# Kernel optimization log

Hardware: AMD Instinct MI355X
Metric: run time of the kernel (lower is better)

The kernel has to match this reference:

```python
import jax, jax.numpy as jnp
import numpy as np

S, I = 512, 384
C_MSA, C_Z, H, C = 64, 128, 8, 32
EPS = 1e-5


def _layernorm(x, g, b):
    mu = jnp.mean(x, axis=-1, keepdims=True)
    var = jnp.var(x, axis=-1, keepdims=True)
    return (x - mu) * jax.lax.rsqrt(var + EPS) * g + b


def setup_inputs() -> dict:
    key = jax.random.key(0)
    ks = jax.random.split(key, 6)
    sc_v = 1.0 / np.sqrt(C_MSA)
    sc_z = 1.0 / np.sqrt(C_Z)
    sc_o = 1.0 / np.sqrt(H * C)
    return {
        "msa_SI": jax.random.normal(ks[0], (S, I, C_MSA), jnp.float32),
        "pair_II": jax.random.normal(ks[1], (I, I, C_Z), jnp.float32),
        "ln_msa_g": jnp.ones((C_MSA,), jnp.float32),
        "ln_msa_b": jnp.zeros((C_MSA,), jnp.float32),
        "ln_pair_g": jnp.ones((C_Z,), jnp.float32),
        "ln_pair_b": jnp.zeros((C_Z,), jnp.float32),
        "W_v": jax.random.normal(ks[2], (C_MSA, H * C), jnp.float32) * sc_v,
        "W_bias": jax.random.normal(ks[3], (C_Z, H), jnp.float32) * sc_z,
        "W_gate": jax.random.normal(ks[4], (C_MSA, H * C), jnp.float32) * sc_v,
        "W_out": jax.random.normal(ks[5], (H * C, C_MSA), jnp.float32) * sc_o,
    }


def reference(msa_SI, pair_II, ln_msa_g, ln_msa_b, ln_pair_g, ln_pair_b,
              W_v, W_bias, W_gate, W_out):
    s, i = msa_SI.shape[:2]
    msa_n = _layernorm(msa_SI, ln_msa_g, ln_msa_b)              # [S,I,Cm]
    v_SIHC = (msa_n @ W_v).reshape(s, i, H, C)                   # [S,I,H,C]
    bias_IIH = _layernorm(pair_II, ln_pair_g, ln_pair_b) @ W_bias  # [I,I,H]
    w_IIH = jax.nn.softmax(bias_IIH, axis=-2)                    # softmax over j
    gate = jax.nn.sigmoid(msa_n @ W_gate)                        # [S,I,H*C]
    # weighted average shared across S: [I,I,H] x [S,I,H,C] -> [S,I,H,C]
    weights = jnp.einsum('ijh,sjhc->sihc', w_IIH, v_SIHC).reshape(s, i, H * C)
    o = gate * weights
    return o @ W_out                                             # [S,I,Cm]
```

## Files before the change

### kernel.cpp

```cpp
#include <hip/hip_runtime.h>
#include <hip/hip_bf16.h>

#define S_DIM 512
#define I_DIM 384
#define CM 64
#define CZ 128
#define H_DIM 8
#define C_DIM 32
#define HC 256
#define II (I_DIM*I_DIM)

typedef short bf16x8 __attribute__((ext_vector_type(8)));
typedef float f32x4 __attribute__((ext_vector_type(4)));

__device__ __forceinline__ float s2f(short s) {
    unsigned int u = ((unsigned int)(unsigned short)s) << 16;
    float f; __builtin_memcpy(&f, &u, 4); return f;
}
__device__ __forceinline__ short f2bf(float f) {
    __hip_bfloat16 h = __float2bfloat16(f);
    short r; __builtin_memcpy(&r, &h, 2); return r;
}

__device__ __forceinline__ void glds16(const short* g, short* l) {
    __builtin_amdgcn_global_load_lds(
        (const __attribute__((address_space(1))) void*)g,
        (__attribute__((address_space(3))) void*)l, 16, 0, 0);
}

__global__ __launch_bounds__(256) void k_pair_ln_bias(
    const float* __restrict__ pair, const float* __restrict__ g,
    const float* __restrict__ b, const float* __restrict__ Wb,
    float* __restrict__ bias)
{
    __shared__ float xs[4][CZ];
    __shared__ float WbT[H_DIM*132];
    const int tid = threadIdx.x;
    const int wv = tid >> 6, lane = tid & 63;
    const int ij = blockIdx.x*4 + wv;

    {
        float4 q = *(const float4*)(Wb + tid*4);
        int m = tid*4;
        WbT[(m&7)*132 + (m>>3)]     = q.x;
        WbT[((m+1)&7)*132 + ((m+1)>>3)] = q.y;
        WbT[((m+2)&7)*132 + ((m+2)>>3)] = q.z;
        WbT[((m+3)&7)*132 + ((m+3)>>3)] = q.w;
    }

    float2 x2 = *(const float2*)(pair + (size_t)ij*CZ + lane*2);
    float s1 = x2.x + x2.y;
    float s2 = x2.x*x2.x + x2.y*x2.y;
#pragma unroll
    for (int off = 32; off > 0; off >>= 1) {
        s1 += __shfl_xor(s1, off, 64);
        s2 += __shfl_xor(s2, off, 64);
    }
    float mu = s1 * (1.f/CZ);
    float var = s2 * (1.f/CZ) - mu*mu;
    float rs = rsqrtf(var + 1e-5f);
    xs[wv][lane*2]   = (x2.x - mu)*rs*g[lane*2]   + b[lane*2];
    xs[wv][lane*2+1] = (x2.y - mu)*rs*g[lane*2+1] + b[lane*2+1];
    __syncthreads();

    const int h = lane >> 3, seg = lane & 7;
    float p = 0.f;
#pragma unroll
    for (int jj = 0; jj < 16; jj++) {
        int c = seg + jj*8;
        p += xs[wv][c] * WbT[h*132 + c];
    }
    p += __shfl_down(p, 4, 64);
    p += __shfl_down(p, 2, 64);
    p += __shfl_down(p, 1, 64);
    if (seg == 0) bias[(size_t)h*II + ij] = p;
}

__global__ __launch_bounds__(384) void k_softmax(
    const float* __restrict__ bias, short* __restrict__ w)
{
    int blk = blockIdx.x;
    int i = blk >> 3, h = blk & 7;
    int j = threadIdx.x;
    float x = bias[(size_t)h*II + i*I_DIM + j];
    float m = x;
#pragma unroll
    for (int off = 32; off > 0; off >>= 1) m = fmaxf(m, __shfl_xor(m, off, 64));
    __shared__ float red[6];
    int wv = j >> 6;
    if ((j & 63) == 0) red[wv] = m;
    __syncthreads();
    m = red[0];
#pragma unroll
    for (int k = 1; k < 6; k++) m = fmaxf(m, red[k]);
    float e = __expf(x - m);
    float s = e;
#pragma unroll
    for (int off = 32; off > 0; off >>= 1) s += __shfl_xor(s, off, 64);
    __syncthreads();
    if ((j & 63) == 0) red[wv] = s;
    __syncthreads();
    s = 0.f;
#pragma unroll
    for (int k = 0; k < 6; k++) s += red[k];
    w[(size_t)h*II + i*I_DIM + j] = f2bf(e / s);
}

__global__ __launch_bounds__(256) void k_prep_w(
    const float* __restrict__ Wv, const float* __restrict__ Wg,
    const float* __restrict__ Wo,
    short* __restrict__ Wt, short* __restrict__ Wot)
{
    int idx = blockIdx.x*256 + threadIdx.x;
    if (idx < 512*64) {
        int n = idx >> 6, k = idx & 63;
        Wt[idx] = f2bf((n < HC) ? Wv[k*HC + n] : Wg[k*HC + (n - HC)]);
    } else {
        int q = idx - 512*64;
        int n = q >> 8, k = q & 255;
        Wot[q] = f2bf(Wo[k*64 + n]);
    }
}

__global__ __launch_bounds__(256) void k4_ln_vgate(
    const float* __restrict__ msa_c,
    const float* __restrict__ gm, const float* __restrict__ bm,
    const short* __restrict__ Wt,
    short* __restrict__ v_t, short* __restrict__ gate)
{
    __shared__ alignas(16) short lds[20992];
    short* As = lds;
    short* Bs = lds + 4608;
    short* T  = lds;

    const int tid = threadIdx.x;
    const int wave = tid >> 6;
    const int lane = tid & 63;
    const int pm = blockIdx.y;

    auto stage_b = [&](int kt) {
#pragma unroll
        for (int c2 = 0; c2 < 8; c2++)
            glds16(Wt + (size_t)(c2*64 + lane)*64 + kt*32 + wave*8,
                   &Bs[(wave*512 + c2*64)*8]);
    };
    stage_b(0);

    {
        const int row = tid >> 2;
        const int seg = tid & 3;
        float xf[16], gf[16], bf[16];
        const float* rp = msa_c + (size_t)(pm*64 + row)*CM + seg*16;
#pragma unroll
        for (int q = 0; q < 4; q++) {
            float4 a = *(const float4*)(rp + q*4);
            xf[q*4] = a.x; xf[q*4+1] = a.y; xf[q*4+2] = a.z; xf[q*4+3] = a.w;
            float4 gg = *(const float4*)(gm + seg*16 + q*4);
            gf[q*4] = gg.x; gf[q*4+1] = gg.y; gf[q*4+2] = gg.z; gf[q*4+3] = gg.w;
            float4 bb = *(const float4*)(bm + seg*16 + q*4);
            bf[q*4] = bb.x; bf[q*4+1] = bb.y; bf[q*4+2] = bb.z; bf[q*4+3] = bb.w;
        }
        float s1 = 0.f, s2 = 0.f;
#pragma unroll
        for (int j = 0; j < 16; j++) { s1 += xf[j]; s2 += xf[j]*xf[j]; }
        s1 += __shfl_xor(s1, 1); s2 += __shfl_xor(s2, 1);
        s1 += __shfl_xor(s1, 2); s2 += __shfl_xor(s2, 2);
        float mu = s1 * (1.f/64.f);
        float var = s2 * (1.f/64.f) - mu*mu;
        float rs = rsqrtf(var + 1e-5f);
        bf16x8 o0, o1;
#pragma unroll
        for (int j = 0; j < 8; j++) {
            o0[j] = f2bf((xf[j]   - mu)*rs*gf[j]   + bf[j]);
            o1[j] = f2bf((xf[8+j] - mu)*rs*gf[8+j] + bf[8+j]);
        }
        *(bf16x8*)&As[row*72 + seg*16]     = o0;
        *(bf16x8*)&As[row*72 + seg*16 + 8] = o1;
    }

    const int fr = lane & 15, fq = lane >> 4;
    f32x4 acc[4][8] = {};

    for (int kt = 0; kt < 2; ++kt) {
        __syncthreads();

        bf16x8 af[4], bfrag[8];
#pragma unroll
        for (int mi = 0; mi < 4; mi++)
            af[mi] = *(const bf16x8*)&As[(mi*16 + fr)*72 + kt*32 + fq*8];
#pragma unroll
        for (int ni = 0; ni < 8; ni++)
            bfrag[ni] = *(const bf16x8*)&Bs[(fq*512 + wave*128 + ni*16 + fr)*8];
#pragma unroll
        for (int mi = 0; mi < 4; mi++)
#pragma unroll
            for (int ni = 0; ni < 8; ni++)
                acc[mi][ni] = __builtin_amdgcn_mfma_f32_16x16x32_bf16(
                    af[mi], bfrag[ni], acc[mi][ni], 0, 0, 0);
        __syncthreads();
        if (kt == 0) stage_b(1);
    }

    const int s_local = pm / 6;
    const int j0 = (pm % 6) * 64;
    if (wave < 2) {
#pragma unroll
        for (int mi = 0; mi < 4; mi++)
#pragma unroll
        for (int ni = 0; ni < 8; ni++) {
            int cl = wave*128 + ni*16 + fr;
            short4 pk;
            pk.x = f2bf(acc[mi][ni][0]);
            pk.y = f2bf(acc[mi][ni][1]);
            pk.z = f2bf(acc[mi][ni][2]);
            pk.w = f2bf(acc[mi][ni][3]);
            *(short4*)&T[cl*72 + mi*16 + fq*4] = pk;
        }
    } else {
#pragma unroll
        for (int mi = 0; mi < 4; mi++)
#pragma unroll
        for (int ni = 0; ni < 8; ni++)
#pragma unroll
        for (int r = 0; r < 4; r++) {
            int rowg = pm*64 + mi*16 + fq*4 + r;
            int col = (wave - 2)*128 + ni*16 + fr;
            gate[(size_t)rowg*HC + col] =
                f2bf(1.f/(1.f + __expf(-acc[mi][ni][r])));
        }
    }
    __syncthreads();
#pragma unroll
    for (int p = 0; p < 8; p++) {
        int unit = p*256 + tid;
        int cl = unit >> 3, part = unit & 7;
        bf16x8 d = *(const bf16x8*)&T[cl*72 + part*8];
        int h = cl >> 5, cc = cl & 31;
        *(bf16x8*)&v_t[(((size_t)s_local*H_DIM + h)*C_DIM + cc)*I_DIM + j0 + part*8] = d;
    }
}

__global__ __launch_bounds__(256, 2) void k56_einsum_proj(
    const short* __restrict__ w,
    const short* __restrict__ v_t,
    const short* __restrict__ gate,
    const short* __restrict__ Wot,
    float* __restrict__ out)
{
    __shared__ alignas(16) short Ws[2][4*192*8];
    __shared__ alignas(16) short Vs[2][2][1024];
    __shared__ alignas(16) short Ob[4][96*40];
    const int tid = threadIdx.x;
    const int wave = tid >> 6, lane = tid & 63;
    const int fr = lane & 15, fq = lane >> 4;
    const int ibase = blockIdx.x * 192;
    const int sp = blockIdx.y;
    const int ms = wave >> 1;
    const int kv = wave & 1;
    const int s  = sp*2 + ms;
    const int iw = kv * 96;

    const short* vbm = v_t + (size_t)s * H_DIM * C_DIM * I_DIM;

    auto stage = [&](int h_, int kt_, int buf) {
        const short* wp = w + (size_t)h_*II + kt_*32 + wave*8;
#pragma unroll
        for (int rg = 0; rg < 3; rg++)
            glds16(wp + (size_t)(ibase + rg*64 + lane)*I_DIM,
                   &Ws[buf][(wave*192 + rg*64)*8]);
        glds16(vbm + (size_t)h_*C_DIM*I_DIM + (lane & 31)*I_DIM + kt_*32
                   + (2*kv + (lane >> 5))*8,
               &Vs[buf][ms][kv*512]);
    };

    f32x4 acc_o[6][4] = {};

    stage(0, 0, 0);
    stage(0, 1, 1);

    for (int h = 0; h < H_DIM; h++) {
        f32x4 acc_e[2][6] = {};
        short4 gv[2][6];
        bf16x8 bw[4];
#pragma unroll
        for (int kt = 0; kt < 12; kt++) {
            const int cb = kt & 1;
            asm volatile("s_waitcnt vmcnt(4)" ::: "memory");
            __builtin_amdgcn_s_barrier();
            __builtin_amdgcn_sched_barrier(0);

            bf16x8 av[2], bwv[6];
#pragma unroll
            for (int mi = 0; mi < 2; mi++)
                av[mi] = *(const bf16x8*)&Vs[cb][ms][(fq*32 + mi*16 + fr)*8];
#pragma unroll
            for (int ni = 0; ni < 6; ni++)
                bwv[ni] = *(const bf16x8*)&Ws[cb][(fq*192 + iw + ni*16 + fr)*8];
            asm volatile("s_waitcnt lgkmcnt(0)" ::: "memory");
            __builtin_amdgcn_s_barrier();
            __builtin_amdgcn_sched_barrier(0);

            if (kt == 10) {
#pragma unroll
                for (int ni = 0; ni < 4; ni++)
                    bw[ni] = *(const bf16x8*)&Wot[(ni*16 + fr)*HC + h*C_DIM + fq*8];
#pragma unroll
                for (int mi = 0; mi < 2; mi++)
#pragma unroll
                for (int ni = 0; ni < 6; ni++)
                    gv[mi][ni] = *(const short4*)&gate[
                        (size_t)(s*I_DIM + ibase + iw + ni*16 + fr)*HC
                        + h*C_DIM + mi*16 + fq*4];
            }
            if (kt < 10)          stage(h, kt + 2, cb);
            else if (h < 7)       stage(h + 1, kt - 10, cb);

            __builtin_amdgcn_s_setprio(1);
#pragma unroll
            for (int mi = 0; mi < 2; mi++)
#pragma unroll
                for (int ni = 0; ni < 6; ni++)
                    acc_e[mi][ni] = __builtin_amdgcn_mfma_f32_16x16x32_bf16(
                        av[mi], bwv[ni], acc_e[mi][ni], 0, 0, 0);
            __builtin_amdgcn_s_setprio(0);
        }

        short* myOb = Ob[wave];
#pragma unroll
        for (int mi = 0; mi < 2; mi++)
#pragma unroll
        for (int ni = 0; ni < 6; ni++) {
            int row = ni*16 + fr;
            int c0 = mi*16 + fq*4;
            short4 g = gv[mi][ni];
            short4 pk;
            pk.x = f2bf(acc_e[mi][ni][0] * s2f(g.x));
            pk.y = f2bf(acc_e[mi][ni][1] * s2f(g.y));
            pk.z = f2bf(acc_e[mi][ni][2] * s2f(g.z));
            pk.w = f2bf(acc_e[mi][ni][3] * s2f(g.w));
            *(short4*)&myOb[row*40 + c0] = pk;
        }
        bf16x8 ao[6];
#pragma unroll
        for (int mi = 0; mi < 6; mi++)
            ao[mi] = *(const bf16x8*)&myOb[(mi*16 + fr)*40 + fq*8];
        __builtin_amdgcn_s_setprio(1);
#pragma unroll
        for (int mi = 0; mi < 6; mi++)
#pragma unroll
            for (int ni = 0; ni < 4; ni++)
                acc_o[mi][ni] = __builtin_amdgcn_mfma_f32_16x16x32_bf16(
                    ao[mi], bw[ni], acc_o[mi][ni], 0, 0, 0);
        __builtin_amdgcn_s_setprio(0);
    }

#pragma unroll
    for (int mi = 0; mi < 6; mi++)
#pragma unroll
    for (int ni = 0; ni < 4; ni++)
#pragma unroll
    for (int r = 0; r < 4; r++) {
        int i = ibase + iw + mi*16 + fq*4 + r;
        int n = ni*16 + fr;
        out[(size_t)(s*I_DIM + i)*CM + n] = acc_o[mi][ni][r];
    }
}

extern "C" void kernel_launch(void* const* d_in, const int* in_sizes, int n_in,
                              void* d_out, int out_size, void* d_ws, size_t ws_size,
                              hipStream_t stream)
{
    const float* msa  = (const float*)d_in[0];
    const float* pair = (const float*)d_in[1];
    const float* gm   = (const float*)d_in[2];
    const float* bm   = (const float*)d_in[3];
    const float* gp   = (const float*)d_in[4];
    const float* bp   = (const float*)d_in[5];
    const float* Wv   = (const float*)d_in[6];
    const float* Wb   = (const float*)d_in[7];
    const float* Wg   = (const float*)d_in[8];
    const float* Wo   = (const float*)d_in[9];

    char* ws = (char*)d_ws;
    short* w    = (short*)ws;
    short* Wt   = (short*)(ws + 2359296);
    short* Wot  = (short*)(ws + 2424832);
    char*  region = ws + 2457600;
    float* bias = (float*)region;

    size_t avail = (ws_size > 2457600u) ? (ws_size - 2457600u) : 0;
    int Sc = 8;
    const int scs[7] = {512, 256, 128, 64, 32, 16, 8};
    for (int i = 0; i < 7; i++) {
        size_t need = (size_t)scs[i] * 393216u;
        if (need < 4718592u) need = 4718592u;
        if (need <= avail) { Sc = scs[i]; break; }
    }
    const int NC = S_DIM / Sc;
    short* v_t  = (short*)region;
    short* gate = (short*)(region + (size_t)Sc*196608u);

    k_pair_ln_bias<<<dim3(II/4), dim3(256), 0, stream>>>(pair, gp, bp, Wb, bias);
    k_prep_w<<<dim3(192), dim3(256), 0, stream>>>(Wv, Wg, Wo, Wt, Wot);
    k_softmax<<<dim3(I_DIM*H_DIM), dim3(I_DIM), 0, stream>>>(bias, w);

    for (int c = 0; c < NC; c++) {
        size_t in_off = (size_t)c * Sc * I_DIM * CM;

        k4_ln_vgate<<<dim3(1, Sc*6, 1), dim3(256), 0, stream>>>(
            msa + in_off, gm, bm, Wt, v_t, gate);

        k56_einsum_proj<<<dim3(2, Sc/2), dim3(256), 0, stream>>>(
            w, v_t, gate, Wot, (float*)d_out + in_off);
    }
}
```

Measured before the change: 460.5 us.

## Restructure einsum kernel: 512-thread blocks, triple-buffered swizzled W, direct V loads

The einsum/projection kernel now uses 512-thread blocks covering four S rows, so each staged tile of the softmax weights w is shared by twice as many waves. The w staging moves to a triple-buffered XOR-swizzled LDS layout, and V fragments are loaded straight from global memory into registers two steps ahead instead of through LDS. Gate and Wout loads move after the k-loop, and the gating epilogue runs in smaller chunks to cut the Ob LDS footprint. The LN/vgate kernel also changes its B staging layout to load inside the k-loop. The hand-set vmcnt waits must exactly match the issue order, and the larger blocks may lower occupancy.

```diff
diff --git a/kernel.cpp b/kernel.cpp
--- a/kernel.cpp
+++ b/kernel.cpp
@@ -138,14 +138,6 @@
     const int lane = tid & 63;
     const int pm = blockIdx.y;
 
-    auto stage_b = [&](int kt) {
-#pragma unroll
-        for (int c2 = 0; c2 < 8; c2++)
-            glds16(Wt + (size_t)(c2*64 + lane)*64 + kt*32 + wave*8,
-                   &Bs[(wave*512 + c2*64)*8]);
-    };
-    stage_b(0);
-
     {
         const int row = tid >> 2;
         const int seg = tid & 3;
@@ -178,10 +170,16 @@
         *(bf16x8*)&As[row*72 + seg*16 + 8] = o1;
     }
 
+    const int lr = lane >> 2, lq = lane & 3;
     const int fr = lane & 15, fq = lane >> 4;
     f32x4 acc[4][8] = {};
 
     for (int kt = 0; kt < 2; ++kt) {
+#pragma unroll
+        for (int c2 = 0; c2 < 8; c2++) {
+            int ch = wave + c2*4;
+            glds16(Wt + (ch*16 + lr)*64 + kt*32 + lq*8, &Bs[ch*512]);
+        }
         __syncthreads();
 
         bf16x8 af[4], bfrag[8];
@@ -190,7 +188,7 @@
             af[mi] = *(const bf16x8*)&As[(mi*16 + fr)*72 + kt*32 + fq*8];
 #pragma unroll
         for (int ni = 0; ni < 8; ni++)
-            bfrag[ni] = *(const bf16x8*)&Bs[(fq*512 + wave*128 + ni*16 + fr)*8];
+            bfrag[ni] = *(const bf16x8*)&Bs[(wave*128 + ni*16 + fr)*32 + fq*8];
 #pragma unroll
         for (int mi = 0; mi < 4; mi++)
 #pragma unroll
@@ -198,7 +196,6 @@
                 acc[mi][ni] = __builtin_amdgcn_mfma_f32_16x16x32_bf16(
                     af[mi], bfrag[ni], acc[mi][ni], 0, 0, 0);
         __syncthreads();
-        if (kt == 0) stage_b(1);
     }
 
     const int s_local = pm / 6;
@@ -240,80 +237,99 @@
     }
 }
 
-__global__ __launch_bounds__(256, 2) void k56_einsum_proj(
+__global__ __launch_bounds__(512, 2) void k56_einsum_proj(
     const short* __restrict__ w,
     const short* __restrict__ v_t,
     const short* __restrict__ gate,
     const short* __restrict__ Wot,
     float* __restrict__ out)
 {
-    __shared__ alignas(16) short Ws[2][4*192*8];
-    __shared__ alignas(16) short Vs[2][2][1024];
-    __shared__ alignas(16) short Ob[4][96*40];
+    __shared__ alignas(16) short Ws[3][192*32];
+    __shared__ alignas(16) short Ob[8][32*40];
     const int tid = threadIdx.x;
     const int wave = tid >> 6, lane = tid & 63;
     const int fr = lane & 15, fq = lane >> 4;
     const int ibase = blockIdx.x * 192;
-    const int sp = blockIdx.y;
+    const int sg = blockIdx.y;
     const int ms = wave >> 1;
     const int kv = wave & 1;
-    const int s  = sp*2 + ms;
+    const int s  = sg*4 + ms;
     const int iw = kv * 96;
 
-    const short* vbm = v_t + (size_t)s * H_DIM * C_DIM * I_DIM;
+    const short* vts = v_t + (size_t)s * H_DIM * C_DIM * I_DIM;
 
     auto stage = [&](int h_, int kt_, int buf) {
-        const short* wp = w + (size_t)h_*II + kt_*32 + wave*8;
-#pragma unroll
-        for (int rg = 0; rg < 3; rg++)
-            glds16(wp + (size_t)(ibase + rg*64 + lane)*I_DIM,
-                   &Ws[buf][(wave*192 + rg*64)*8]);
-        glds16(vbm + (size_t)h_*C_DIM*I_DIM + (lane & 31)*I_DIM + kt_*32
-                   + (2*kv + (lane >> 5))*8,
-               &Vs[buf][ms][kv*512]);
+        const short* base = w + (size_t)h_*II + (size_t)kt_*32;
+        {
+            int row = wave*16 + (lane >> 2);
+            int q = (lane & 3) ^ ((row >> 1) & 3);
+            glds16(base + (size_t)(ibase + row)*I_DIM + q*8,
+                   &Ws[buf][wave*16*32]);
+        }
+        if (wave < 4) {
+            int row = (8 + wave)*16 + (lane >> 2);
+            int q = (lane & 3) ^ ((row >> 1) & 3);
+            glds16(base + (size_t)(ibase + row)*I_DIM + q*8,
+                   &Ws[buf][(8 + wave)*16*32]);
+        }
     };
+    auto loadAv = [&](bf16x8* d, int h_, int kt_) {
+        const short* vb = vts + (size_t)h_*(C_DIM*I_DIM) + kt_*32;
+        d[0] = *(const bf16x8*)&vb[fr*I_DIM + fq*8];
+        d[1] = *(const bf16x8*)&vb[(16 + fr)*I_DIM + fq*8];
+    };
 
     f32x4 acc_o[6][4] = {};
-
+    bf16x8 avs[3][2];
+
+    loadAv(avs[0], 0, 0);
+    loadAv(avs[1], 0, 1);
+    __builtin_amdgcn_sched_barrier(0);
     stage(0, 0, 0);
     stage(0, 1, 1);
-
+    stage(0, 2, 2);
+    __builtin_amdgcn_sched_barrier(0);
+
+#pragma unroll 1
     for (int h = 0; h < H_DIM; h++) {
         f32x4 acc_e[2][6] = {};
-        short4 gv[2][6];
-        bf16x8 bw[4];
 #pragma unroll
         for (int kt = 0; kt < 12; kt++) {
-            const int cb = kt & 1;
-            asm volatile("s_waitcnt vmcnt(4)" ::: "memory");
+            const int cb = kt % 3;
+            if (h == 0 && kt == 0) {
+                if (wave < 4) asm volatile("s_waitcnt vmcnt(4)" ::: "memory");
+                else          asm volatile("s_waitcnt vmcnt(2)" ::: "memory");
+            } else if (h == 7 && kt == 10) {
+                if (wave < 4) asm volatile("s_waitcnt vmcnt(4)" ::: "memory");
+                else          asm volatile("s_waitcnt vmcnt(3)" ::: "memory");
+            } else if (h == 7 && kt == 11) {
+                asm volatile("s_waitcnt vmcnt(0)" ::: "memory");
+            } else {
+                if (wave < 4) asm volatile("s_waitcnt vmcnt(6)" ::: "memory");
+                else          asm volatile("s_waitcnt vmcnt(4)" ::: "memory");
+            }
             __builtin_amdgcn_s_barrier();
             __builtin_amdgcn_sched_barrier(0);
 
-            bf16x8 av[2], bwv[6];
-#pragma unroll
-            for (int mi = 0; mi < 2; mi++)
-                av[mi] = *(const bf16x8*)&Vs[cb][ms][(fq*32 + mi*16 + fr)*8];
-#pragma unroll
-            for (int ni = 0; ni < 6; ni++)
-                bwv[ni] = *(const bf16x8*)&Ws[cb][(fq*192 + iw + ni*16 + fr)*8];
+            bf16x8 bwv[6];
+#pragma unroll
+            for (int ni = 0; ni < 6; ni++) {
+                int row = iw + ni*16 + fr;
+                bwv[ni] = *(const bf16x8*)
+                    &Ws[cb][row*32 + ((fq ^ ((row >> 1) & 3)) << 3)];
+            }
+            if (kt < 10)      loadAv(avs[(kt+2)%3], h, kt + 2);
+            else if (h < 7)   loadAv(avs[(kt+2)%3], h + 1, kt - 10);
+            __builtin_amdgcn_sched_barrier(0);
+
             asm volatile("s_waitcnt lgkmcnt(0)" ::: "memory");
+            __builtin_amdgcn_sched_barrier(0);
             __builtin_amdgcn_s_barrier();
             __builtin_amdgcn_sched_barrier(0);
 
-            if (kt == 10) {
-#pragma unroll
-                for (int ni = 0; ni < 4; ni++)
-                    bw[ni] = *(const bf16x8*)&Wot[(ni*16 + fr)*HC + h*C_DIM + fq*8];
-#pragma unroll
-                for (int mi = 0; mi < 2; mi++)
-#pragma unroll
-                for (int ni = 0; ni < 6; ni++)
-                    gv[mi][ni] = *(const short4*)&gate[
-                        (size_t)(s*I_DIM + ibase + iw + ni*16 + fr)*HC
-                        + h*C_DIM + mi*16 + fq*4];
-            }
-            if (kt < 10)          stage(h, kt + 2, cb);
-            else if (h < 7)       stage(h + 1, kt - 10, cb);
+            if (kt < 9)       stage(h, kt + 3, cb);
+            else if (h < 7)   stage(h + 1, kt - 9, cb);
+            __builtin_amdgcn_sched_barrier(0);
 
             __builtin_amdgcn_s_setprio(1);
 #pragma unroll
@@ -321,37 +337,53 @@
 #pragma unroll
                 for (int ni = 0; ni < 6; ni++)
                     acc_e[mi][ni] = __builtin_amdgcn_mfma_f32_16x16x32_bf16(
-                        av[mi], bwv[ni], acc_e[mi][ni], 0, 0, 0);
+                        avs[cb][mi], bwv[ni], acc_e[mi][ni], 0, 0, 0);
             __builtin_amdgcn_s_setprio(0);
         }
 
+        bf16x8 bw[4];
+#pragma unroll
+        for (int ni = 0; ni < 4; ni++)
+            bw[ni] = *(const bf16x8*)&Wot[(ni*16 + fr)*HC + h*C_DIM + fq*8];
+        short4 gv[2][6];
+#pragma unroll
+        for (int mi = 0; mi < 2; mi++)
+#pragma unroll
+        for (int ni = 0; ni < 6; ni++)
+            gv[mi][ni] = *(const short4*)&gate[
+                (size_t)(s*I_DIM + ibase + iw + ni*16 + fr)*HC
+                + h*C_DIM + mi*16 + fq*4];
+
         short* myOb = Ob[wave];
 #pragma unroll
-        for (int mi = 0; mi < 2; mi++)
-#pragma unroll
-        for (int ni = 0; ni < 6; ni++) {
-            int row = ni*16 + fr;
-            int c0 = mi*16 + fq*4;
-            short4 g = gv[mi][ni];
-            short4 pk;
-            pk.x = f2bf(acc_e[mi][ni][0] * s2f(g.x));
-            pk.y = f2bf(acc_e[mi][ni][1] * s2f(g.y));
-            pk.z = f2bf(acc_e[mi][ni][2] * s2f(g.z));
-            pk.w = f2bf(acc_e[mi][ni][3] * s2f(g.w));
-            *(short4*)&myOb[row*40 + c0] = pk;
-        }
-        bf16x8 ao[6];
-#pragma unroll
-        for (int mi = 0; mi < 6; mi++)
-            ao[mi] = *(const bf16x8*)&myOb[(mi*16 + fr)*40 + fq*8];
-        __builtin_amdgcn_s_setprio(1);
-#pragma unroll
-        for (int mi = 0; mi < 6; mi++)
-#pragma unroll
-            for (int ni = 0; ni < 4; ni++)
-                acc_o[mi][ni] = __builtin_amdgcn_mfma_f32_16x16x32_bf16(
-                    ao[mi], bw[ni], acc_o[mi][ni], 0, 0, 0);
-        __builtin_amdgcn_s_setprio(0);
+        for (int p = 0; p < 3; p++) {
+#pragma unroll
+            for (int t = 0; t < 2; t++) {
+                int ni = p*2 + t;
+#pragma unroll
+                for (int mi = 0; mi < 2; mi++) {
+                    short4 g = gv[mi][ni];
+                    short4 pk;
+                    pk.x = f2bf(acc_e[mi][ni][0] * s2f(g.x));
+                    pk.y = f2bf(acc_e[mi][ni][1] * s2f(g.y));
+                    pk.z = f2bf(acc_e[mi][ni][2] * s2f(g.z));
+                    pk.w = f2bf(acc_e[mi][ni][3] * s2f(g.w));
+                    *(short4*)&myOb[(t*16 + fr)*40 + mi*16 + fq*4] = pk;
+                }
+            }
+            bf16x8 ao[2];
+#pragma unroll
+            for (int t = 0; t < 2; t++)
+                ao[t] = *(const bf16x8*)&myOb[(t*16 + fr)*40 + fq*8];
+            __builtin_amdgcn_s_setprio(1);
+#pragma unroll
+            for (int t = 0; t < 2; t++)
+#pragma unroll
+                for (int ni = 0; ni < 4; ni++)
+                    acc_o[p*2 + t][ni] = __builtin_amdgcn_mfma_f32_16x16x32_bf16(
+                        ao[t], bw[ni], acc_o[p*2 + t][ni], 0, 0, 0);
+            __builtin_amdgcn_s_setprio(0);
+        }
     }
 
 #pragma unroll
@@ -410,7 +442,7 @@
         k4_ln_vgate<<<dim3(1, Sc*6, 1), dim3(256), 0, stream>>>(
             msa + in_off, gm, bm, Wt, v_t, gate);
 
-        k56_einsum_proj<<<dim3(2, Sc/2), dim3(256), 0, stream>>>(
+        k56_einsum_proj<<<dim3(2, Sc/4), dim3(512), 0, stream>>>(
             w, v_t, gate, Wot, (float*)d_out + in_off);
     }
 }
```

Result: faster. 411.2 us (-10.7%).
